# Kernel optimization log

Measured on AMD Instinct MI355X. Metric: run time of the kernel, lower is better.

Reference implementation:

```python
import jax, jax.numpy as jnp
import numpy as np

DIM = 256
WINDOW = 512  # look_backward=1, look_forward=0, causal


def setup_inputs() -> dict:
    key = jax.random.key(0)
    ks = jax.random.split(key, 7)
    B, N, D = 8, 8192, DIM
    s = D ** -0.5
    return {
        "x": jax.random.normal(ks[0], (B, D, N), dtype=jnp.float32),
        "Wq": jax.random.normal(ks[1], (D, D), dtype=jnp.float32) * s,
        "bq": jax.random.normal(ks[2], (D,), dtype=jnp.float32) * 0.01,
        "Wk": jax.random.normal(ks[3], (D, D), dtype=jnp.float32) * s,
        "bk": jax.random.normal(ks[4], (D,), dtype=jnp.float32) * 0.01,
        "Wv": jax.random.normal(ks[5], (D, D), dtype=jnp.float32) * s,
        "bv": jax.random.normal(ks[6], (D,), dtype=jnp.float32) * 0.01,
    }


def _local_attention(q, k, v, window):
    # q,k,v: (B, N, D); causal sliding-window attention, look_backward=1 window.
    b, n, d = q.shape
    nw = n // window  # N assumed multiple of window (autopad no-op here)
    scale = d ** -0.5
    qb = q.reshape(b, nw, window, d)
    kb = k.reshape(b, nw, window, d)
    vb = v.reshape(b, nw, window, d)

    def look_back(t):
        prev = jnp.pad(t, ((0, 0), (1, 0), (0, 0), (0, 0)))[:, :-1]
        return jnp.concatenate([prev, t], axis=2)  # (b, nw, 2*window, d)

    kb2 = look_back(kb)
    vb2 = look_back(vb)

    pos = jnp.arange(n).reshape(nw, window)
    prev_pos = jnp.pad(pos, ((1, 0), (0, 0)), constant_values=-1)[:-1]
    kpos = jnp.concatenate([prev_pos, pos], axis=1)  # (nw, 2*window)
    # causal mask + mask out the (nonexistent) window before window 0
    mask = (pos[:, :, None] >= kpos[:, None, :]) & (kpos[:, None, :] >= 0)

    scores = jnp.einsum('bnqd,bnkd->bnqk', qb, kb2) * scale
    scores = jnp.where(mask[None], scores, jnp.asarray(-1e9, scores.dtype))
    attn = jax.nn.softmax(scores, axis=-1)  # dropout(0.1) omitted: eval mode
    out = jnp.einsum('bnqk,bnkd->bnqd', attn, vb2)
    return out.reshape(b, n, d)


def reference(x, Wq, bq, Wk, bk, Wv, bv):
    # x: (B, D, N) -> permute -> (B, N, D)
    xp = jnp.transpose(x, (0, 2, 1))
    q = xp @ Wq.T + bq
    k = xp @ Wk.T + bk
    v = xp @ Wv.T + bv
    y = xp + _local_attention(q, k, v, WINDOW)  # residual
    return jnp.transpose(y, (0, 2, 1))
```

## Files before the change

kernel.cpp:

```cpp
#include <hip/hip_runtime.h>
#include <hip/hip_bf16.h>

#define DIM  256
#define NSEQ 8192
#define BATCH 8
#define WIN  512

typedef __attribute__((ext_vector_type(8))) short short8;
typedef __attribute__((ext_vector_type(4))) float floatx4;

union PFU { int i[4]; short8 v; };

__device__ __forceinline__ int packbf(float a, float b) {
    __hip_bfloat162 h;
    h.x = __float2bfloat16(a);
    h.y = __float2bfloat16(b);
    int r;
    __builtin_memcpy(&r, &h, 4);
    return r;
}

__device__ __forceinline__ void gld_lds16(void* lds_dst, const void* g_src) {
    __builtin_amdgcn_global_load_lds(
        (const __attribute__((address_space(1))) void*)g_src,
        (__attribute__((address_space(3))) void*)lds_dst,
        16, 0, 0);
}

__global__ __launch_bounds__(256) void k_transpose(const float* __restrict__ x,
                                                   __hip_bfloat16* __restrict__ xT) {
    __shared__ float tile[64][65];
    const int b  = blockIdx.z;
    const int n0 = blockIdx.x * 64;
    const int d0 = blockIdx.y * 64;
    const int t  = threadIdx.x;
    const int ln = t & 63, grp = t >> 6;

    const float* xb = x + (size_t)b * DIM * NSEQ;
#pragma unroll
    for (int i = 0; i < 16; ++i) {
        int d = grp * 16 + i;
        tile[d][ln] = xb[(size_t)(d0 + d) * NSEQ + n0 + ln];
    }
    __syncthreads();
    __hip_bfloat16* xTb = xT + (size_t)b * NSEQ * DIM;
#pragma unroll
    for (int i = 0; i < 16; ++i) {
        int n = grp * 16 + i;
        xTb[(size_t)(n0 + n) * DIM + d0 + ln] = __float2bfloat16(tile[ln][n]);
    }
}

__global__ __launch_bounds__(256) void k_wcast(const float* __restrict__ w0,
                                               const float* __restrict__ w1,
                                               const float* __restrict__ w2,
                                               __hip_bfloat16* __restrict__ wb) {
    int i = (blockIdx.x * 256 + threadIdx.x) * 4;
    const float* s = (i < 65536) ? (w0 + i) : ((i < 131072) ? (w1 + i - 65536) : (w2 + i - 131072));
    float4 v = *(const float4*)s;
    union { __hip_bfloat16 h[4]; ushort4 u; } cv;
    cv.h[0] = __float2bfloat16(v.x);
    cv.h[1] = __float2bfloat16(v.y);
    cv.h[2] = __float2bfloat16(v.z);
    cv.h[3] = __float2bfloat16(v.w);
    *(ushort4*)(wb + i) = cv.u;
}

__global__ __launch_bounds__(256) void k_proj(const __hip_bfloat16* __restrict__ xT,
                                              const __hip_bfloat16* __restrict__ wb,
                                              const float* __restrict__ bq,
                                              const float* __restrict__ bk,
                                              const float* __restrict__ bv,
                                              __hip_bfloat16* __restrict__ qo,
                                              __hip_bfloat16* __restrict__ ko,
                                              __hip_bfloat16* __restrict__ vto) {
    __shared__ __hip_bfloat16 As[4096];
    __shared__ __hip_bfloat16 Bs[4096];

    const int mode = blockIdx.y;
    const int b    = blockIdx.z;
    const int xb   = blockIdx.x;
    const int tid  = threadIdx.x;
    const int wv   = tid >> 6;
    const int l    = tid & 63;
    const int qd   = l >> 4;
    const int lm   = l & 15;
    const int wm   = (wv & 1) * 64;
    const int wn   = (wv >> 1) * 64;

    int m0, n0;
    const __hip_bfloat16 *Ap, *Bp;
    const __hip_bfloat16* xTb = xT + (size_t)b * NSEQ * DIM;
    if (mode < 2) {
        m0 = (xb >> 1) * 128;  n0 = (xb & 1) * 128;
        Ap = xTb + (size_t)m0 * DIM;
        Bp = wb + mode * 65536 + (size_t)n0 * DIM;
    } else {
        m0 = (xb & 1) * 128;   n0 = (xb >> 1) * 128;
        Ap = wb + 2 * 65536 + (size_t)m0 * DIM;
        Bp = xTb + (size_t)n0 * DIM;
    }

    floatx4 acc[4][4];
#pragma unroll
    for (int i = 0; i < 4; ++i)
#pragma unroll
        for (int j = 0; j < 4; ++j) acc[i][j] = (floatx4){0.f, 0.f, 0.f, 0.f};

    for (int k0 = 0; k0 < DIM; k0 += 32) {
#pragma unroll
        for (int r = 0; r < 2; ++r) {
            int row = r * 64 + (tid >> 2);
            int seg = (tid & 3) * 8;
            gld_lds16((char*)As + r * 4096 + wv * 1024, Ap + (size_t)row * DIM + k0 + seg);
            gld_lds16((char*)Bs + r * 4096 + wv * 1024, Bp + (size_t)row * DIM + k0 + seg);
        }
        __syncthreads();
        short8 af[4], bfv[4];
#pragma unroll
        for (int mt = 0; mt < 4; ++mt)
            af[mt] = *(const short8*)(As + (wm + mt * 16 + lm) * 32 + qd * 8);
#pragma unroll
        for (int nt = 0; nt < 4; ++nt)
            bfv[nt] = *(const short8*)(Bs + (wn + nt * 16 + lm) * 32 + qd * 8);
#pragma unroll
        for (int mt = 0; mt < 4; ++mt)
#pragma unroll
            for (int nt = 0; nt < 4; ++nt)
                acc[mt][nt] = __builtin_amdgcn_mfma_f32_16x16x32_bf16(af[mt], bfv[nt], acc[mt][nt], 0, 0, 0);
        __syncthreads();
    }

    const float* bias = (mode == 0) ? bq : ((mode == 1) ? bk : bv);
    __hip_bfloat16* op;
    size_t ostr;
    if (mode == 0)      { op = qo  + (size_t)b * NSEQ * DIM; ostr = DIM; }
    else if (mode == 1) { op = ko  + (size_t)b * NSEQ * DIM; ostr = DIM; }
    else                { op = vto + (size_t)b * DIM * NSEQ; ostr = NSEQ; }

    float bc[4];
    if (mode < 2) {
#pragma unroll
        for (int nt = 0; nt < 4; ++nt) bc[nt] = bias[n0 + wn + nt * 16 + lm];
    }
#pragma unroll
    for (int mt = 0; mt < 4; ++mt)
#pragma unroll
        for (int nt = 0; nt < 4; ++nt)
#pragma unroll
            for (int r = 0; r < 4; ++r) {
                int row = wm + mt * 16 + qd * 4 + r;
                int col = wn + nt * 16 + lm;
                float bb = (mode < 2) ? bc[nt] : bias[m0 + row];
                op[(size_t)(m0 + row) * ostr + n0 + col] = __float2bfloat16(acc[mt][nt][r] + bb);
            }
}

__global__ __launch_bounds__(512, 2) void k_attn(const __hip_bfloat16* __restrict__ qm,
                                                 const __hip_bfloat16* __restrict__ km,
                                                 const __hip_bfloat16* __restrict__ vtm,
                                                 const float* __restrict__ x,
                                                 float* __restrict__ out) {
    __shared__ __align__(16) char kbuf[2][16384];
    __shared__ __align__(16) char vbuf[2][16384];

    const int w  = blockIdx.x, b = blockIdx.y, qt = blockIdx.z;
    const int tid = threadIdx.x;
    const int wv = tid >> 6;
    const int l  = tid & 63;
    const int m  = l & 15;
    const int qd = l >> 4;

    const int qbw   = qt * 256 + wv * 32;
    const int koff0 = w * WIN - WIN;

    short8 qf[2][8];
#pragma unroll
    for (int u = 0; u < 2; ++u) {
        const __hip_bfloat16* qrow =
            qm + ((size_t)b * NSEQ + (size_t)(w * WIN + qbw + u * 16 + m)) * DIM;
#pragma unroll
        for (int s = 0; s < 8; ++s)
            qf[u][s] = *(const short8*)(qrow + s * 32 + qd * 8);
    }

    const char* kbase = (const char*)(km + (size_t)b * NSEQ * DIM);
    const char* vbase = (const char*)(vtm + (size_t)b * DIM * NSEQ);

    const int c0  = (w == 0) ? 16 : 0;
    const int c1w = (512 + qbw + 63) >> 5;
    const int c1b = (799 + qt * 256) >> 5;

    const bool   isK     = wv < 4;
    const size_t gstride = isK ? (size_t)64 : (size_t)16 * NSEQ * 2;
    const size_t adv     = isK ? (size_t)32 * 512 : (size_t)64;
    const int    lbase   = (isK ? wv * 4 : (wv - 4) * 4) * 1024 + l * 16;
    const char* gp0;
    if (isK)
        gp0 = kbase + (size_t)(koff0 + c0 * 32 + (wv >> 1) * 16 + m) * 512 +
              (size_t)((wv & 1) * 16 + qd) * 16;
    else
        gp0 = vbase + (size_t)((wv - 4) * 64 + m) * (NSEQ * 2) +
              (size_t)(koff0 + c0 * 32) * 2 + (size_t)qd * 16;

    floatx4 o[2][16];
#pragma unroll
    for (int u = 0; u < 2; ++u)
#pragma unroll
        for (int t = 0; t < 16; ++t) o[u][t] = (floatx4){0.f, 0.f, 0.f, 0.f};
    float mi[2] = {-INFINITY, -INFINITY};
    float li[2] = {0.f, 0.f};
    const float sscale = 0.0625f * 1.4426950408889634f;

    const int a0 = (((qd & 1) * 2) * 16 + m) * 4;
    const int a1 = a0 + 64;
    const bool hi = (qd >> 1) != 0;

    int4 rg[4];
#pragma unroll
    for (int i = 0; i < 4; ++i)
        rg[i] = *(const int4*)(gp0 + (size_t)i * gstride);
    gp0 += adv;
    {
        char* d0 = (isK ? kbuf[0] : vbuf[0]) + lbase;
#pragma unroll
        for (int i = 0; i < 4; ++i)
            *(int4*)(d0 + i * 1024) = rg[i];
    }
    __syncthreads();

    int pb = 0;
    for (int c = c0; c < c1b; ++c) {
        const bool more = (c + 1 < c1b);
        if (more) {
#pragma unroll
            for (int i = 0; i < 4; ++i)
                rg[i] = *(const int4*)(gp0 + (size_t)i * gstride);
            gp0 += adv;
        }
        if (c < c1w) {
            const char* kbp = kbuf[pb];
            floatx4 st[2][2];
#pragma unroll
            for (int u = 0; u < 2; ++u)
#pragma unroll
                for (int t = 0; t < 2; ++t) st[u][t] = (floatx4){0.f, 0.f, 0.f, 0.f};
            __builtin_amdgcn_s_setprio(1);
#pragma unroll
            for (int t = 0; t < 2; ++t)
#pragma unroll
                for (int s = 0; s < 8; ++s) {
                    short8 kf = *(const short8*)(kbp + ((t * 8 + s) * 64 + l) * 16);
                    st[0][t] = __builtin_amdgcn_mfma_f32_16x16x32_bf16(kf, qf[0][s], st[0][t], 0, 0, 0);
                    st[1][t] = __builtin_amdgcn_mfma_f32_16x16x32_bf16(kf, qf[1][s], st[1][t], 0, 0, 0);
                }
            __builtin_amdgcn_s_setprio(0);
            const int kl0 = c * 32;
            short8 pf[2];
#pragma unroll
            for (int u = 0; u < 2; ++u) {
                const int lim = 512 + qbw + u * 16 + m;
                const bool needmask = (kl0 + 31) > lim;
                float p[8];
#pragma unroll
                for (int t = 0; t < 2; ++t)
#pragma unroll
                    for (int r = 0; r < 4; ++r) {
                        float v = st[u][t][r] * sscale;
                        if (needmask) {
                            int key = kl0 + t * 16 + qd * 4 + r;
                            v = (key <= lim) ? v : -INFINITY;
                        }
                        p[t * 4 + r] = v;
                    }
                float mx = p[0];
#pragma unroll
                for (int i = 1; i < 8; ++i) mx = fmaxf(mx, p[i]);
                mx = fmaxf(mx, __shfl_xor(mx, 16, 64));
                mx = fmaxf(mx, __shfl_xor(mx, 32, 64));
                float mnew;
                if (__all(mx <= mi[u] + 8.0f)) mnew = mi[u];
                else                           mnew = fmaxf(mi[u], mx);
                const float alpha = exp2f(mi[u] - mnew);
                float ps = 0.f;
#pragma unroll
                for (int i = 0; i < 8; ++i) { p[i] = exp2f(p[i] - mnew); ps += p[i]; }
                ps += __shfl_xor(ps, 16, 64);
                ps += __shfl_xor(ps, 32, 64);
                li[u] = li[u] * alpha + ps;
                mi[u] = mnew;
                if (!__all(alpha == 1.0f)) {
#pragma unroll
                    for (int t = 0; t < 16; ++t) {
                        o[u][t][0] *= alpha; o[u][t][1] *= alpha;
                        o[u][t][2] *= alpha; o[u][t][3] *= alpha;
                    }
                }
                int pd0 = packbf(p[0], p[1]);
                int pd1 = packbf(p[2], p[3]);
                int pd2 = packbf(p[4], p[5]);
                int pd3 = packbf(p[6], p[7]);
                int x0 = __builtin_amdgcn_ds_bpermute(a0, pd0);
                int y0 = __builtin_amdgcn_ds_bpermute(a0, pd2);
                int x1 = __builtin_amdgcn_ds_bpermute(a0, pd1);
                int y1 = __builtin_amdgcn_ds_bpermute(a0, pd3);
                int x2 = __builtin_amdgcn_ds_bpermute(a1, pd0);
                int y2 = __builtin_amdgcn_ds_bpermute(a1, pd2);
                int x3 = __builtin_amdgcn_ds_bpermute(a1, pd1);
                int y3 = __builtin_amdgcn_ds_bpermute(a1, pd3);
                PFU pu;
                pu.i[0] = hi ? y0 : x0;
                pu.i[1] = hi ? y1 : x1;
                pu.i[2] = hi ? y2 : x2;
                pu.i[3] = hi ? y3 : x3;
                pf[u] = pu.v;
            }
            const char* vbp = vbuf[pb];
            __builtin_amdgcn_s_setprio(1);
#pragma unroll
            for (int t = 0; t < 16; ++t) {
                short8 vf = *(const short8*)(vbp + (t * 64 + l) * 16);
                o[0][t] = __builtin_amdgcn_mfma_f32_16x16x32_bf16(vf, pf[0], o[0][t], 0, 0, 0);
                o[1][t] = __builtin_amdgcn_mfma_f32_16x16x32_bf16(vf, pf[1], o[1][t], 0, 0, 0);
            }
            __builtin_amdgcn_s_setprio(0);
        }
        if (more) {
            char* dst = (isK ? kbuf[pb ^ 1] : vbuf[pb ^ 1]) + lbase;
#pragma unroll
            for (int i = 0; i < 4; ++i)
                *(int4*)(dst + i * 1024) = rg[i];
        }
        __syncthreads();
        pb ^= 1;
    }

#pragma unroll
    for (int u = 0; u < 2; ++u) {
        const float inv = 1.f / li[u];
        const int ng = w * WIN + qbw + u * 16 + m;
        const float* xr  = x   + (size_t)b * DIM * NSEQ + ng;
        float*       orw = out + (size_t)b * DIM * NSEQ + ng;
#pragma unroll
        for (int t = 0; t < 16; ++t)
#pragma unroll
            for (int r = 0; r < 4; ++r) {
                int d = t * 16 + qd * 4 + r;
                orw[(size_t)d * NSEQ] = xr[(size_t)d * NSEQ] + o[u][t][r] * inv;
            }
    }
}

extern "C" void kernel_launch(void* const* d_in, const int* in_sizes, int n_in,
                              void* d_out, int out_size, void* d_ws, size_t ws_size,
                              hipStream_t stream) {
    const float* x  = (const float*)d_in[0];
    const float* Wq = (const float*)d_in[1];
    const float* bq = (const float*)d_in[2];
    const float* Wk = (const float*)d_in[3];
    const float* bk = (const float*)d_in[4];
    const float* Wv = (const float*)d_in[5];
    const float* bv = (const float*)d_in[6];

    char* ws = (char*)d_ws;
    const size_t SZ = (size_t)BATCH * NSEQ * DIM * sizeof(__hip_bfloat16);
    __hip_bfloat16* xT  = (__hip_bfloat16*)(ws);
    __hip_bfloat16* qb_ = (__hip_bfloat16*)(ws + SZ);
    __hip_bfloat16* kb_ = (__hip_bfloat16*)(ws + 2 * SZ);
    __hip_bfloat16* vt_ = (__hip_bfloat16*)(ws + 3 * SZ);
    __hip_bfloat16* wb_ = (__hip_bfloat16*)(ws + 4 * SZ);

    k_transpose<<<dim3(NSEQ / 64, DIM / 64, BATCH), 256, 0, stream>>>(x, xT);
    k_wcast<<<dim3(192), 256, 0, stream>>>(Wq, Wk, Wv, wb_);
    k_proj<<<dim3(128, 3, BATCH), 256, 0, stream>>>(xT, wb_, bq, bk, bv, qb_, kb_, vt_);
    k_attn<<<dim3(16, BATCH, 2), 512, 0, stream>>>(qb_, kb_, vt_, x, (float*)d_out);
}
```

Baseline: 352.0 us.

## Fuse Q/K/V projections per row tile with full-K LDS staging of x

The projection kernel now loads a 64-row tile of transposed x (full 256-wide K) into LDS once and computes all three Q, K and V projections from it. Weight fragments are read directly from global memory rather than staged through LDS. This removes re-reading xT three times and drops the per-K-step barriers. The transpose kernel also now writes packed 4-element bf16 stores instead of scalar ones. The cost is larger LDS use per block and uncached direct global weight reads.

```diff
diff --git a/kernel.cpp b/kernel.cpp
--- a/kernel.cpp
+++ b/kernel.cpp
@@ -44,10 +44,15 @@
     }
     __syncthreads();
     __hip_bfloat16* xTb = xT + (size_t)b * NSEQ * DIM;
-#pragma unroll
-    for (int i = 0; i < 16; ++i) {
-        int n = grp * 16 + i;
-        xTb[(size_t)(n0 + n) * DIM + d0 + ln] = __float2bfloat16(tile[ln][n]);
+    const int a2 = t & 15, nr = t >> 4;
+#pragma unroll
+    for (int i = 0; i < 4; ++i) {
+        const int n = i * 16 + nr;
+        union { __hip_bfloat16 h[4]; ushort4 u; } pk;
+#pragma unroll
+        for (int k = 0; k < 4; ++k)
+            pk.h[k] = __float2bfloat16(tile[a2 * 4 + k][n]);
+        *(ushort4*)(xTb + (size_t)(n0 + n) * DIM + d0 + a2 * 4) = pk.u;
     }
 }
 
@@ -66,94 +71,96 @@
     *(ushort4*)(wb + i) = cv.u;
 }
 
-__global__ __launch_bounds__(256) void k_proj(const __hip_bfloat16* __restrict__ xT,
-                                              const __hip_bfloat16* __restrict__ wb,
-                                              const float* __restrict__ bq,
-                                              const float* __restrict__ bk,
-                                              const float* __restrict__ bv,
-                                              __hip_bfloat16* __restrict__ qo,
-                                              __hip_bfloat16* __restrict__ ko,
-                                              __hip_bfloat16* __restrict__ vto) {
-    __shared__ __hip_bfloat16 As[4096];
-    __shared__ __hip_bfloat16 Bs[4096];
-
-    const int mode = blockIdx.y;
-    const int b    = blockIdx.z;
-    const int xb   = blockIdx.x;
-    const int tid  = threadIdx.x;
-    const int wv   = tid >> 6;
-    const int l    = tid & 63;
-    const int qd   = l >> 4;
-    const int lm   = l & 15;
-    const int wm   = (wv & 1) * 64;
-    const int wn   = (wv >> 1) * 64;
-
-    int m0, n0;
-    const __hip_bfloat16 *Ap, *Bp;
-    const __hip_bfloat16* xTb = xT + (size_t)b * NSEQ * DIM;
-    if (mode < 2) {
-        m0 = (xb >> 1) * 128;  n0 = (xb & 1) * 128;
-        Ap = xTb + (size_t)m0 * DIM;
-        Bp = wb + mode * 65536 + (size_t)n0 * DIM;
-    } else {
-        m0 = (xb & 1) * 128;   n0 = (xb >> 1) * 128;
-        Ap = wb + 2 * 65536 + (size_t)m0 * DIM;
-        Bp = xTb + (size_t)n0 * DIM;
-    }
-
-    floatx4 acc[4][4];
-#pragma unroll
-    for (int i = 0; i < 4; ++i)
-#pragma unroll
-        for (int j = 0; j < 4; ++j) acc[i][j] = (floatx4){0.f, 0.f, 0.f, 0.f};
-
-    for (int k0 = 0; k0 < DIM; k0 += 32) {
-#pragma unroll
-        for (int r = 0; r < 2; ++r) {
-            int row = r * 64 + (tid >> 2);
-            int seg = (tid & 3) * 8;
-            gld_lds16((char*)As + r * 4096 + wv * 1024, Ap + (size_t)row * DIM + k0 + seg);
-            gld_lds16((char*)Bs + r * 4096 + wv * 1024, Bp + (size_t)row * DIM + k0 + seg);
-        }
-        __syncthreads();
-        short8 af[4], bfv[4];
-#pragma unroll
-        for (int mt = 0; mt < 4; ++mt)
-            af[mt] = *(const short8*)(As + (wm + mt * 16 + lm) * 32 + qd * 8);
-#pragma unroll
-        for (int nt = 0; nt < 4; ++nt)
-            bfv[nt] = *(const short8*)(Bs + (wn + nt * 16 + lm) * 32 + qd * 8);
-#pragma unroll
-        for (int mt = 0; mt < 4; ++mt)
-#pragma unroll
-            for (int nt = 0; nt < 4; ++nt)
-                acc[mt][nt] = __builtin_amdgcn_mfma_f32_16x16x32_bf16(af[mt], bfv[nt], acc[mt][nt], 0, 0, 0);
-        __syncthreads();
-    }
-
-    const float* bias = (mode == 0) ? bq : ((mode == 1) ? bk : bv);
-    __hip_bfloat16* op;
-    size_t ostr;
-    if (mode == 0)      { op = qo  + (size_t)b * NSEQ * DIM; ostr = DIM; }
-    else if (mode == 1) { op = ko  + (size_t)b * NSEQ * DIM; ostr = DIM; }
-    else                { op = vto + (size_t)b * DIM * NSEQ; ostr = NSEQ; }
-
-    float bc[4];
-    if (mode < 2) {
-#pragma unroll
-        for (int nt = 0; nt < 4; ++nt) bc[nt] = bias[n0 + wn + nt * 16 + lm];
-    }
-#pragma unroll
-    for (int mt = 0; mt < 4; ++mt)
-#pragma unroll
-        for (int nt = 0; nt < 4; ++nt)
-#pragma unroll
-            for (int r = 0; r < 4; ++r) {
-                int row = wm + mt * 16 + qd * 4 + r;
-                int col = wn + nt * 16 + lm;
-                float bb = (mode < 2) ? bc[nt] : bias[m0 + row];
-                op[(size_t)(m0 + row) * ostr + n0 + col] = __float2bfloat16(acc[mt][nt][r] + bb);
+__global__ __launch_bounds__(256, 3) void k_proj(const __hip_bfloat16* __restrict__ xT,
+                                                 const __hip_bfloat16* __restrict__ wb,
+                                                 const float* __restrict__ bq,
+                                                 const float* __restrict__ bk,
+                                                 const float* __restrict__ bv,
+                                                 __hip_bfloat16* __restrict__ qo,
+                                                 __hip_bfloat16* __restrict__ ko,
+                                                 __hip_bfloat16* __restrict__ vto) {
+    __shared__ __align__(16) char As[32768];
+    const int b   = blockIdx.y;
+    const int m0  = blockIdx.x * 64;
+    const int tid = threadIdx.x;
+    const int wv  = tid >> 6;
+    const int l   = tid & 63;
+    const int lm  = l & 15;
+    const int qd  = l >> 4;
+    const int wn  = wv * 64;
+
+    const char* Ap = (const char*)(xT + ((size_t)b * NSEQ + m0) * DIM);
+#pragma unroll
+    for (int ii = 0; ii < 8; ++ii) {
+        const int ks = wv * 2 + (ii >> 2);
+        const int r0 = (ii & 3) * 16;
+        gld_lds16(As + ks * 4096 + r0 * 64,
+                  Ap + (size_t)(r0 + (l >> 2)) * 512 + ks * 64 + (l & 3) * 16);
+    }
+    __syncthreads();
+
+#pragma unroll
+    for (int mode = 0; mode < 3; ++mode) {
+        const __hip_bfloat16* wp = wb + mode * 65536;
+        floatx4 acc[4][4];
+#pragma unroll
+        for (int i = 0; i < 4; ++i)
+#pragma unroll
+            for (int j = 0; j < 4; ++j) acc[i][j] = (floatx4){0.f, 0.f, 0.f, 0.f};
+
+#pragma unroll
+        for (int ks = 0; ks < 8; ++ks) {
+            short8 wf[4], af[4];
+#pragma unroll
+            for (int j = 0; j < 4; ++j)
+                wf[j] = *(const short8*)(wp + (size_t)(wn + j * 16 + lm) * DIM + ks * 32 + qd * 8);
+#pragma unroll
+            for (int j = 0; j < 4; ++j)
+                af[j] = *(const short8*)(As + ks * 4096 + (j * 16 + lm) * 64 + qd * 16);
+            if (mode < 2) {
+#pragma unroll
+                for (int mt = 0; mt < 4; ++mt)
+#pragma unroll
+                    for (int nt = 0; nt < 4; ++nt)
+                        acc[mt][nt] = __builtin_amdgcn_mfma_f32_16x16x32_bf16(af[mt], wf[nt], acc[mt][nt], 0, 0, 0);
+            } else {
+#pragma unroll
+                for (int jw = 0; jw < 4; ++jw)
+#pragma unroll
+                    for (int ja = 0; ja < 4; ++ja)
+                        acc[jw][ja] = __builtin_amdgcn_mfma_f32_16x16x32_bf16(wf[jw], af[ja], acc[jw][ja], 0, 0, 0);
             }
+        }
+
+        if (mode < 2) {
+            const float* bias = mode ? bk : bq;
+            __hip_bfloat16* op = (mode ? ko : qo) + (size_t)b * NSEQ * DIM;
+            float bc[4];
+#pragma unroll
+            for (int nt = 0; nt < 4; ++nt) bc[nt] = bias[wn + nt * 16 + lm];
+#pragma unroll
+            for (int mt = 0; mt < 4; ++mt)
+#pragma unroll
+                for (int nt = 0; nt < 4; ++nt)
+#pragma unroll
+                    for (int r = 0; r < 4; ++r)
+                        op[(size_t)(m0 + mt * 16 + qd * 4 + r) * DIM + wn + nt * 16 + lm] =
+                            __float2bfloat16(acc[mt][nt][r] + bc[nt]);
+        } else {
+            __hip_bfloat16* op = vto + (size_t)b * DIM * NSEQ;
+#pragma unroll
+            for (int jw = 0; jw < 4; ++jw)
+#pragma unroll
+                for (int r = 0; r < 4; ++r) {
+                    const int d = wn + jw * 16 + qd * 4 + r;
+                    const float bb = bv[d];
+#pragma unroll
+                    for (int ja = 0; ja < 4; ++ja)
+                        op[(size_t)d * NSEQ + m0 + ja * 16 + lm] =
+                            __float2bfloat16(acc[jw][ja][r] + bb);
+                }
+        }
+    }
 }
 
 __global__ __launch_bounds__(512, 2) void k_attn(const __hip_bfloat16* __restrict__ qm,
@@ -372,6 +379,6 @@
 
     k_transpose<<<dim3(NSEQ / 64, DIM / 64, BATCH), 256, 0, stream>>>(x, xT);
     k_wcast<<<dim3(192), 256, 0, stream>>>(Wq, Wk, Wv, wb_);
-    k_proj<<<dim3(128, 3, BATCH), 256, 0, stream>>>(xT, wb_, bq, bk, bv, qb_, kb_, vt_);
+    k_proj<<<dim3(NSEQ / 64, BATCH), 256, 0, stream>>>(xT, wb_, bq, bk, bv, qb_, kb_, vt_);
     k_attn<<<dim3(16, BATCH, 2), 512, 0, stream>>>(qb_, kb_, vt_, x, (float*)d_out);
 }
```

Measured after the change: 357.5 us. About the same (+1.6%).
